# Performance work log

Measured on AMD Instinct MI355X. Metric: run time of the kernel, lower is better.

Reference implementation:

```python
import jax, jax.numpy as jnp
import numpy as np

S, B, H = 2048, 2, 1024
NH = 16
HD = H // NH  # 64


def setup_inputs() -> dict:
    key = jax.random.key(0)
    k1, k2 = jax.random.split(key)
    hidden_states = jax.random.normal(k1, (S, B, H), dtype=jnp.float32)
    W_qkv = jax.random.normal(k2, (3 * H, H), dtype=jnp.float32) * (H ** -0.5)
    b_qkv = jnp.zeros((3 * H,), dtype=jnp.float32)
    return {"hidden_states": hidden_states, "W_qkv": W_qkv, "b_qkv": b_qkv}


def reference(hidden_states, W_qkv, b_qkv):
    s, b, h = hidden_states.shape
    # QKV projection: [S,B,3H] -> [S,B,NH,3*HD] -> split
    qkv = hidden_states @ W_qkv.T + b_qkv
    qkv = qkv.reshape(s, b, NH, 3 * HD)
    q, k, v = jnp.split(qkv, 3, axis=-1)  # each [S,B,NH,HD]
    norm_factor = HD ** -0.5
    # scores: [B,NH,Sq,Sk]
    scores = jnp.einsum('sbhd,tbhd->bhst', q, k) * norm_factor
    # Cumsum sequence-op (seq_op_in_fp32=True): cumsum over key dim, scaled by Sq^-0.5
    probs = jnp.cumsum(scores.astype(jnp.float32), axis=-1) * (s ** -0.5)
    probs = probs.astype(hidden_states.dtype)
    # PV: [B,NH,Sq,HD] -> seq-first [Sq,B,NH*HD]
    ctx = jnp.einsum('bhst,tbhd->sbhd', probs, v)
    return ctx.reshape(s, b, h)
```

## Files before the change

### kernel.cpp

```cpp
#include <hip/hip_runtime.h>

#define S 2048
#define B 2
#define H 1024
#define NH 16
#define HD 64
#define THREE_H 3072
#define ROWS (S*B)

typedef __attribute__((ext_vector_type(8))) short short8;
typedef __attribute__((ext_vector_type(4))) float f32x4;
typedef const __attribute__((address_space(1))) unsigned int* gptr_t;
typedef __attribute__((address_space(3))) unsigned int* lptr_t;

#define N8_A (ROWS * H / 8)
#define N8_W (THREE_H * H / 8)

__device__ __forceinline__ ushort f2bf(float f) {
    union { float f; unsigned u; } v; v.f = f;
    unsigned r = v.u + 0x7fffu + ((v.u >> 16) & 1u);
    return (ushort)(r >> 16);
}
__device__ __forceinline__ float bf2f(ushort u) {
    union { unsigned u; float f; } v; v.u = ((unsigned)u) << 16;
    return v.f;
}

__global__ void cast_both(const float* __restrict__ A, const float* __restrict__ W,
                          ushort* __restrict__ Ab, ushort* __restrict__ Wb) {
    int i = blockIdx.x * 256 + threadIdx.x;
    const float4* s4;
    ushort* dst;
    if (i < N8_A) { s4 = (const float4*)A; dst = Ab; }
    else if (i < N8_A + N8_W) { s4 = (const float4*)W; dst = Wb; i -= N8_A; }
    else return;
    float4 a = s4[2 * i], b = s4[2 * i + 1];
    short8 o;
    o[0] = f2bf(a.x); o[1] = f2bf(a.y); o[2] = f2bf(a.z); o[3] = f2bf(a.w);
    o[4] = f2bf(b.x); o[5] = f2bf(b.y); o[6] = f2bf(b.z); o[7] = f2bf(b.w);
    *(short8*)(dst + 8 * (size_t)i) = o;
}

__global__ __launch_bounds__(512) void qkv_gemm_mfma(const ushort* __restrict__ Abf,
                                                     const ushort* __restrict__ Wbf,
                                                     const float* __restrict__ bias,
                                                     ushort* __restrict__ Qb,
                                                     ushort* __restrict__ Ktd,
                                                     ushort* __restrict__ Vtd) {
    __shared__ ushort Abuf[128 * 32];
    __shared__ ushort Bbuf[128 * 32];
    const int tid = threadIdx.x;
    const int wave = tid >> 6, lane = tid & 63;
    const int wr = wave >> 1, wc = wave & 1;
    const int row0 = blockIdx.x * 128;
    const int col0 = blockIdx.y * 128;

    f32x4 acc[2][4] = {};

    const int lrow = lane >> 2;
    const int gk = ((lane & 3) ^ ((lrow >> 1) & 3)) * 8;
    const int il = lane & 15, ko = lane >> 4;

    for (int k0 = 0; k0 < H; k0 += 32) {
        {
            int row = wave * 16 + lrow;
            __builtin_amdgcn_global_load_lds(
                (gptr_t)&Abf[(size_t)(row0 + row) * H + k0 + gk],
                (lptr_t)&Abuf[wave * 512 + lane * 8], 16, 0, 0);
            __builtin_amdgcn_global_load_lds(
                (gptr_t)&Wbf[(size_t)(col0 + row) * H + k0 + gk],
                (lptr_t)&Bbuf[wave * 512 + lane * 8], 16, 0, 0);
        }
        __syncthreads();

        short8 af[2], bfr[4];
#pragma unroll
        for (int m = 0; m < 2; ++m) {
            int ar = wr * 32 + m * 16 + il;
            af[m] = *(const short8*)&Abuf[ar * 32 + (ko ^ ((ar >> 1) & 3)) * 8];
        }
#pragma unroll
        for (int n = 0; n < 4; ++n) {
            int br = wc * 64 + n * 16 + il;
            bfr[n] = *(const short8*)&Bbuf[br * 32 + (ko ^ ((br >> 1) & 3)) * 8];
        }
#pragma unroll
        for (int m = 0; m < 2; ++m)
#pragma unroll
            for (int n = 0; n < 4; ++n)
                acc[m][n] = __builtin_amdgcn_mfma_f32_16x16x32_bf16(af[m], bfr[n], acc[m][n], 0, 0, 0);
        __syncthreads();
    }

#pragma unroll
    for (int n = 0; n < 4; ++n) {
        int cbase = col0 + wc * 64 + n * 16;
        int h   = cbase / 192;
        int r3  = cbase % 192;
        int sel = r3 >> 6;
        int d   = (r3 & 63) + il;
        float bv = bias[cbase + il];
        if (sel == 0) {
#pragma unroll
            for (int m = 0; m < 2; ++m) {
                int rowb = row0 + wr * 32 + m * 16 + ko * 4;
#pragma unroll
                for (int j = 0; j < 4; ++j) {
                    int r = rowb + j;
                    int s = r >> 1, b = r & 1;
                    Qb[((size_t)((b * NH + h) * S + s)) * HD + d] = f2bf(acc[m][n][j] + bv);
                }
            }
        } else {
            ushort* dst = (sel == 1) ? Ktd : Vtd;
            const size_t ro0 = ((size_t)(h)      * HD + d) * S;
            const size_t ro1 = ((size_t)(NH + h) * HD + d) * S;
#pragma unroll
            for (int m = 0; m < 2; ++m) {
                int t0 = (row0 + wr * 32 + m * 16 + ko * 4) >> 1;
                uint lo = (uint)f2bf(acc[m][n][0] + bv) |
                          ((uint)f2bf(acc[m][n][2] + bv) << 16);
                uint hi = (uint)f2bf(acc[m][n][1] + bv) |
                          ((uint)f2bf(acc[m][n][3] + bv) << 16);
                *(uint*)&dst[ro0 + t0] = lo;
                *(uint*)&dst[ro1 + t0] = hi;
            }
        }
    }
}

__global__ __launch_bounds__(256) void vscan(ushort* __restrict__ Vtd) {
    const int row = blockIdx.x * 4 + (threadIdx.x >> 6);
    const int lane = threadIdx.x & 63;
    ushort* vp = Vtd + (size_t)row * S + lane * 32;
    float v[32];
#pragma unroll
    for (int q = 0; q < 4; ++q) {
        short8 x = *(const short8*)(vp + q * 8);
#pragma unroll
        for (int k = 0; k < 8; ++k) v[q * 8 + k] = bf2f((ushort)x[k]);
    }
    float sum = 0.f;
#pragma unroll
    for (int k = 0; k < 32; ++k) sum += v[k];
    float t = sum;
#pragma unroll
    for (int off = 1; off < 64; off <<= 1) {
        float o = __shfl_down(t, off, 64);
        if (lane + off < 64) t += o;
    }
    float acc = t - sum;
#pragma unroll
    for (int k = 31; k >= 0; --k) { acc += v[k]; v[k] = acc; }
#pragma unroll
    for (int q = 0; q < 4; ++q) {
        short8 o;
#pragma unroll
        for (int k = 0; k < 8; ++k) o[k] = f2bf(v[q * 8 + k]);
        *(short8*)(vp + q * 8) = o;
    }
}

__global__ __launch_bounds__(256) void kvm_mfma(const ushort* __restrict__ Kt,
                                                const ushort* __restrict__ Vt,
                                                float* __restrict__ Mpart) {
    __shared__ float red[2][4096];
    const int bh = blockIdx.x, kb = blockIdx.y;
    const int tid = threadIdx.x, wave = tid >> 6, lane = tid & 63;
    const int slice = kb * 4 + wave;
    const ushort* Kp = Kt + (size_t)bh * HD * S;
    const ushort* Vp = Vt + (size_t)bh * HD * S;
    f32x4 acc[4][4] = {};
    const int il = lane & 15, g = lane >> 4;
    const int tbase = slice * 128 + g * 8;
#pragma unroll
    for (int ks = 0; ks < 4; ++ks) {
        const int t = tbase + ks * 32;
        short8 af[4], bfv[4];
#pragma unroll
        for (int m = 0; m < 4; ++m) af[m]  = *(const short8*)&Kp[(size_t)(m * 16 + il) * S + t];
#pragma unroll
        for (int n = 0; n < 4; ++n) bfv[n] = *(const short8*)&Vp[(size_t)(n * 16 + il) * S + t];
#pragma unroll
        for (int m = 0; m < 4; ++m)
#pragma unroll
            for (int n = 0; n < 4; ++n)
                acc[m][n] = __builtin_amdgcn_mfma_f32_16x16x32_bf16(af[m], bfv[n], acc[m][n], 0, 0, 0);
    }
#define DUMP(dstbuf)                                                        \
    { float* _d = (dstbuf);                                                 \
      _Pragma("unroll") for (int m = 0; m < 4; ++m)                         \
      _Pragma("unroll") for (int n = 0; n < 4; ++n)                         \
      _Pragma("unroll") for (int j = 0; j < 4; ++j)                         \
          _d[(m * 16 + g * 4 + j) * 64 + n * 16 + il] = acc[m][n][j]; }
#define ADDIN(srcbuf)                                                       \
    { const float* _s = (srcbuf);                                           \
      _Pragma("unroll") for (int m = 0; m < 4; ++m)                         \
      _Pragma("unroll") for (int n = 0; n < 4; ++n)                         \
      _Pragma("unroll") for (int j = 0; j < 4; ++j)                         \
          acc[m][n][j] += _s[(m * 16 + g * 4 + j) * 64 + n * 16 + il]; }
    if (wave == 1) DUMP(red[0]);
    if (wave == 3) DUMP(red[1]);
    __syncthreads();
    if (wave == 0) ADDIN(red[0]);
    if (wave == 2) ADDIN(red[1]);
    __syncthreads();
    if (wave == 2) DUMP(red[0]);
    __syncthreads();
    if (wave == 0) {
        ADDIN(red[0]);
        float* Mp = Mpart + ((size_t)kb * 32 + bh) * 4096;
#pragma unroll
        for (int m = 0; m < 4; ++m)
#pragma unroll
            for (int n = 0; n < 4; ++n)
#pragma unroll
                for (int j = 0; j < 4; ++j)
                    Mp[(m * 16 + g * 4 + j) * 64 + n * 16 + il] = acc[m][n][j];
    }
#undef DUMP
#undef ADDIN
}

__global__ __launch_bounds__(256) void qm_mfma(const ushort* __restrict__ Qb,
                                               const float* __restrict__ Mpart,
                                               float* __restrict__ out) {
    __shared__ ushort Mt[64][72];
    const int bh = blockIdx.x, b = bh >> 4, h = bh & 15;
    const int tid = threadIdx.x;
    {
        const int i = tid >> 2, jq = (tid & 3) * 16;
        f32x4 s0 = {}, s1 = {}, s2 = {}, s3 = {};
#pragma unroll
        for (int sl = 0; sl < 4; ++sl) {
            const float* p = Mpart + ((size_t)sl * 32 + bh) * 4096 + i * 64 + jq;
            s0 += *(const f32x4*)(p);
            s1 += *(const f32x4*)(p + 4);
            s2 += *(const f32x4*)(p + 8);
            s3 += *(const f32x4*)(p + 12);
        }
#pragma unroll
        for (int k = 0; k < 4; ++k) {
            Mt[jq + 0  + k][i] = f2bf(s0[k]);
            Mt[jq + 4  + k][i] = f2bf(s1[k]);
            Mt[jq + 8  + k][i] = f2bf(s2[k]);
            Mt[jq + 12 + k][i] = f2bf(s3[k]);
        }
    }
    __syncthreads();
    const int wave = tid >> 6, lane = tid & 63;
    const int sl15 = lane & 15, koct = (lane >> 4) * 8;
    const int s0b = blockIdx.y * 256 + wave * 64;
    f32x4 acc[4][4] = {};
#pragma unroll
    for (int ks = 0; ks < 2; ++ks) {
        short8 af[4], bfv[4];
#pragma unroll
        for (int m = 0; m < 4; ++m) {
            int s = s0b + m * 16 + sl15;
            af[m] = *(const short8*)&Qb[((size_t)bh * S + s) * HD + ks * 32 + koct];
        }
#pragma unroll
        for (int n = 0; n < 4; ++n)
            bfv[n] = *(const short8*)&Mt[n * 16 + sl15][ks * 32 + koct];
#pragma unroll
        for (int m = 0; m < 4; ++m)
#pragma unroll
            for (int n = 0; n < 4; ++n)
                acc[m][n] = __builtin_amdgcn_mfma_f32_16x16x32_bf16(af[m], bfv[n], acc[m][n], 0, 0, 0);
    }
    const float scale = 0.125f * 0.02209708691207961f;
#pragma unroll
    for (int m = 0; m < 4; ++m)
#pragma unroll
        for (int n = 0; n < 4; ++n)
#pragma unroll
            for (int j = 0; j < 4; ++j) {
                int s = s0b + m * 16 + (lane >> 4) * 4 + j;
                int d = n * 16 + sl15;
                out[(size_t)(s * B + b) * H + h * 64 + d] = acc[m][n][j] * scale;
            }
}

extern "C" void kernel_launch(void* const* d_in, const int* in_sizes, int n_in,
                              void* d_out, int out_size, void* d_ws, size_t ws_size,
                              hipStream_t stream) {
    const float* hidden = (const float*)d_in[0];
    const float* W      = (const float*)d_in[1];
    const float* bias   = (const float*)d_in[2];
    float* out = (float*)d_out;

    ushort* Qb    = (ushort*)d_ws;
    ushort* Ktd   = Qb + 4194304;
    ushort* Vtd   = Ktd + 4194304;
    float*  Mpart = (float*)(Vtd + 4194304);
    ushort* Abf   = (ushort*)(Mpart + 524288);
    ushort* Wbf   = Abf + 4194304;

    cast_both<<<(N8_A + N8_W + 255) / 256, 256, 0, stream>>>(hidden, W, Abf, Wbf);
    qkv_gemm_mfma<<<dim3(ROWS / 128, THREE_H / 128), 512, 0, stream>>>(Abf, Wbf, bias, Qb, Ktd, Vtd);
    vscan<<<512, 256, 0, stream>>>(Vtd);
    kvm_mfma<<<dim3(32, 4), 256, 0, stream>>>(Ktd, Vtd, Mpart);
    qm_mfma<<<dim3(32, 8), 256, 0, stream>>>(Qb, Mpart, out);
}
```

Before: 70.93 us.

## Double-buffer QKV GEMM LDS tiles with BK=64 and async prefetch

Restructures the QKV projection GEMM main loop to use two LDS buffers with a 64-wide K tile, issuing global-to-LDS loads two stages ahead and waiting with explicit vmcnt counts instead of a full sync each step. The swizzle is changed to an 8-way XOR over the wider rows, and MFMA sections get raised wave priority. This is meant to overlap memory latency with matrix math and halve the number of barriers. In exchange it quadruples the LDS footprint, which may reduce occupancy, and relies on hand-counted waitcnt correctness.

```diff
diff --git a/kernel.cpp b/kernel.cpp
--- a/kernel.cpp
+++ b/kernel.cpp
@@ -47,8 +47,8 @@
                                                      ushort* __restrict__ Qb,
                                                      ushort* __restrict__ Ktd,
                                                      ushort* __restrict__ Vtd) {
-    __shared__ ushort Abuf[128 * 32];
-    __shared__ ushort Bbuf[128 * 32];
+    __shared__ ushort Abuf[2][128 * 64];
+    __shared__ ushort Bbuf[2][128 * 64];
     const int tid = threadIdx.x;
     const int wave = tid >> 6, lane = tid & 63;
     const int wr = wave >> 1, wc = wave & 1;
@@ -57,40 +57,67 @@
 
     f32x4 acc[2][4] = {};
 
-    const int lrow = lane >> 2;
-    const int gk = ((lane & 3) ^ ((lrow >> 1) & 3)) * 8;
+    const int srow = lane >> 3;
+    const int gk = ((lane & 7) ^ srow) * 8;
     const int il = lane & 15, ko = lane >> 4;
 
-    for (int k0 = 0; k0 < H; k0 += 32) {
-        {
-            int row = wave * 16 + lrow;
-            __builtin_amdgcn_global_load_lds(
-                (gptr_t)&Abf[(size_t)(row0 + row) * H + k0 + gk],
-                (lptr_t)&Abuf[wave * 512 + lane * 8], 16, 0, 0);
-            __builtin_amdgcn_global_load_lds(
-                (gptr_t)&Wbf[(size_t)(col0 + row) * H + k0 + gk],
-                (lptr_t)&Bbuf[wave * 512 + lane * 8], 16, 0, 0);
-        }
-        __syncthreads();
-
-        short8 af[2], bfr[4];
-#pragma unroll
-        for (int m = 0; m < 2; ++m) {
-            int ar = wr * 32 + m * 16 + il;
-            af[m] = *(const short8*)&Abuf[ar * 32 + (ko ^ ((ar >> 1) & 3)) * 8];
-        }
-#pragma unroll
-        for (int n = 0; n < 4; ++n) {
-            int br = wc * 64 + n * 16 + il;
-            bfr[n] = *(const short8*)&Bbuf[br * 32 + (ko ^ ((br >> 1) & 3)) * 8];
-        }
-#pragma unroll
-        for (int m = 0; m < 2; ++m)
-#pragma unroll
-            for (int n = 0; n < 4; ++n)
-                acc[m][n] = __builtin_amdgcn_mfma_f32_16x16x32_bf16(af[m], bfr[n], acc[m][n], 0, 0, 0);
-        __syncthreads();
-    }
+    const size_t arow0 = (size_t)(row0 + wave * 16 + srow) * H + gk;
+    const size_t arow1 = arow0 + (size_t)8 * H;
+    const size_t wrow0 = (size_t)(col0 + wave * 16 + srow) * H + gk;
+    const size_t wrow1 = wrow0 + (size_t)8 * H;
+    const int ld0 = (wave * 16) * 64 + lane * 8;
+    const int ld1 = ld0 + 8 * 64;
+
+#define STAGE(buf, k0)                                                        \
+    {                                                                         \
+        __builtin_amdgcn_global_load_lds((gptr_t)&Abf[arow0 + (k0)],          \
+            (lptr_t)&Abuf[buf][ld0], 16, 0, 0);                               \
+        __builtin_amdgcn_global_load_lds((gptr_t)&Wbf[wrow0 + (k0)],          \
+            (lptr_t)&Bbuf[buf][ld0], 16, 0, 0);                               \
+        __builtin_amdgcn_global_load_lds((gptr_t)&Abf[arow1 + (k0)],          \
+            (lptr_t)&Abuf[buf][ld1], 16, 0, 0);                               \
+        __builtin_amdgcn_global_load_lds((gptr_t)&Wbf[wrow1 + (k0)],          \
+            (lptr_t)&Bbuf[buf][ld1], 16, 0, 0);                               \
+    }
+
+    STAGE(0, 0);
+    STAGE(1, 64);
+
+    int cur = 0;
+    for (int t = 0; t < 16; ++t) {
+        if (t < 15) { asm volatile("s_waitcnt vmcnt(4)" ::: "memory"); }
+        else        { asm volatile("s_waitcnt vmcnt(0)" ::: "memory"); }
+        __builtin_amdgcn_s_barrier();
+        __builtin_amdgcn_sched_barrier(0);
+
+#pragma unroll
+        for (int kh = 0; kh < 2; ++kh) {
+            short8 af[2], bfr[4];
+#pragma unroll
+            for (int m = 0; m < 2; ++m) {
+                int ar = wr * 32 + m * 16 + il;
+                af[m] = *(const short8*)&Abuf[cur][ar * 64 + ((kh * 4 + ko) ^ (ar & 7)) * 8];
+            }
+#pragma unroll
+            for (int n = 0; n < 4; ++n) {
+                int br = wc * 64 + n * 16 + il;
+                bfr[n] = *(const short8*)&Bbuf[cur][br * 64 + ((kh * 4 + ko) ^ (br & 7)) * 8];
+            }
+            __builtin_amdgcn_s_setprio(1);
+#pragma unroll
+            for (int m = 0; m < 2; ++m)
+#pragma unroll
+                for (int n = 0; n < 4; ++n)
+                    acc[m][n] = __builtin_amdgcn_mfma_f32_16x16x32_bf16(af[m], bfr[n], acc[m][n], 0, 0, 0);
+            __builtin_amdgcn_s_setprio(0);
+        }
+
+        __builtin_amdgcn_s_barrier();
+        __builtin_amdgcn_sched_barrier(0);
+        if (t < 14) STAGE(cur, (t + 2) * 64);
+        cur ^= 1;
+    }
+#undef STAGE
 
 #pragma unroll
     for (int n = 0; n < 4; ++n) {
```

Result: slower. 75.24 us (+6.1%).

## Fuse fp32-to-bf16 cast into QKV GEMM with register-prefetched global loads

Applied to the files above, without the earlier changes.

Removes the separate cast kernel and its bf16 staging buffers. The GEMM now reads fp32 activations and weights directly, converts them with packed bf16 conversion instructions, and writes them to LDS. The next K-slice is prefetched into registers while the current one is computed, and MFMA priority is raised. The cost is that the GEMM reads twice the bytes per tile, and each W tile is re-read as fp32 by many blocks. The per-iteration conversion and explicit barriers add instruction overhead.

```diff
diff --git a/kernel.cpp b/kernel.cpp
--- a/kernel.cpp
+++ b/kernel.cpp
@@ -10,11 +10,9 @@
 
 typedef __attribute__((ext_vector_type(8))) short short8;
 typedef __attribute__((ext_vector_type(4))) float f32x4;
+typedef __attribute__((ext_vector_type(4))) uint uint4v;
 typedef const __attribute__((address_space(1))) unsigned int* gptr_t;
 typedef __attribute__((address_space(3))) unsigned int* lptr_t;
-
-#define N8_A (ROWS * H / 8)
-#define N8_W (THREE_H * H / 8)
 
 __device__ __forceinline__ ushort f2bf(float f) {
     union { float f; unsigned u; } v; v.f = f;
@@ -25,24 +23,14 @@
     union { unsigned u; float f; } v; v.u = ((unsigned)u) << 16;
     return v.f;
 }
-
-__global__ void cast_both(const float* __restrict__ A, const float* __restrict__ W,
-                          ushort* __restrict__ Ab, ushort* __restrict__ Wb) {
-    int i = blockIdx.x * 256 + threadIdx.x;
-    const float4* s4;
-    ushort* dst;
-    if (i < N8_A) { s4 = (const float4*)A; dst = Ab; }
-    else if (i < N8_A + N8_W) { s4 = (const float4*)W; dst = Wb; i -= N8_A; }
-    else return;
-    float4 a = s4[2 * i], b = s4[2 * i + 1];
-    short8 o;
-    o[0] = f2bf(a.x); o[1] = f2bf(a.y); o[2] = f2bf(a.z); o[3] = f2bf(a.w);
-    o[4] = f2bf(b.x); o[5] = f2bf(b.y); o[6] = f2bf(b.z); o[7] = f2bf(b.w);
-    *(short8*)(dst + 8 * (size_t)i) = o;
-}
-
-__global__ __launch_bounds__(512) void qkv_gemm_mfma(const ushort* __restrict__ Abf,
-                                                     const ushort* __restrict__ Wbf,
+__device__ __forceinline__ uint cvtpk(float lo, float hi) {
+    uint r;
+    asm volatile("v_cvt_pk_bf16_f32 %0, %1, %2" : "=v"(r) : "v"(lo), "v"(hi));
+    return r;
+}
+
+__global__ __launch_bounds__(512) void qkv_gemm_mfma(const float* __restrict__ Af,
+                                                     const float* __restrict__ Wf,
                                                      const float* __restrict__ bias,
                                                      ushort* __restrict__ Qb,
                                                      ushort* __restrict__ Ktd,
@@ -58,20 +46,40 @@
     f32x4 acc[2][4] = {};
 
     const int lrow = lane >> 2;
-    const int gk = ((lane & 3) ^ ((lrow >> 1) & 3)) * 8;
+    const int gko = (lane & 3) ^ ((lrow >> 1) & 3);
     const int il = lane & 15, ko = lane >> 4;
 
-    for (int k0 = 0; k0 < H; k0 += 32) {
+    const float* aP = Af + (size_t)(row0 + wave * 16 + lrow) * H + gko * 8;
+    const float* wP = Wf + (size_t)(col0 + wave * 16 + lrow) * H + gko * 8;
+
+    f32x4 aLo = *(const f32x4*)(aP), aHi = *(const f32x4*)(aP + 4);
+    f32x4 wLo = *(const f32x4*)(wP), wHi = *(const f32x4*)(wP + 4);
+
+    uint* adst = (uint*)&Abuf[wave * 512 + lane * 8];
+    uint* bdst = (uint*)&Bbuf[wave * 512 + lane * 8];
+
+    for (int t = 0; t < 32; ++t) {
+        __builtin_amdgcn_s_barrier();
+        __builtin_amdgcn_sched_barrier(0);
         {
-            int row = wave * 16 + lrow;
-            __builtin_amdgcn_global_load_lds(
-                (gptr_t)&Abf[(size_t)(row0 + row) * H + k0 + gk],
-                (lptr_t)&Abuf[wave * 512 + lane * 8], 16, 0, 0);
-            __builtin_amdgcn_global_load_lds(
-                (gptr_t)&Wbf[(size_t)(col0 + row) * H + k0 + gk],
-                (lptr_t)&Bbuf[wave * 512 + lane * 8], 16, 0, 0);
-        }
-        __syncthreads();
+            uint4v pa, pw;
+            pa.x = cvtpk(aLo.x, aLo.y); pa.y = cvtpk(aLo.z, aLo.w);
+            pa.z = cvtpk(aHi.x, aHi.y); pa.w = cvtpk(aHi.z, aHi.w);
+            pw.x = cvtpk(wLo.x, wLo.y); pw.y = cvtpk(wLo.z, wLo.w);
+            pw.z = cvtpk(wHi.x, wHi.y); pw.w = cvtpk(wHi.z, wHi.w);
+            *(uint4v*)adst = pa;
+            *(uint4v*)bdst = pw;
+        }
+        asm volatile("s_waitcnt lgkmcnt(0)" ::: "memory");
+        if (t < 31) {
+            const float* ap = aP + (t + 1) * 32;
+            const float* wp = wP + (t + 1) * 32;
+            aLo = *(const f32x4*)(ap); aHi = *(const f32x4*)(ap + 4);
+            wLo = *(const f32x4*)(wp); wHi = *(const f32x4*)(wp + 4);
+        }
+        __builtin_amdgcn_sched_barrier(0);
+        __builtin_amdgcn_s_barrier();
+        __builtin_amdgcn_sched_barrier(0);
 
         short8 af[2], bfr[4];
 #pragma unroll
@@ -84,12 +92,13 @@
             int br = wc * 64 + n * 16 + il;
             bfr[n] = *(const short8*)&Bbuf[br * 32 + (ko ^ ((br >> 1) & 3)) * 8];
         }
+        __builtin_amdgcn_s_setprio(1);
 #pragma unroll
         for (int m = 0; m < 2; ++m)
 #pragma unroll
             for (int n = 0; n < 4; ++n)
                 acc[m][n] = __builtin_amdgcn_mfma_f32_16x16x32_bf16(af[m], bfr[n], acc[m][n], 0, 0, 0);
-        __syncthreads();
+        __builtin_amdgcn_s_setprio(0);
     }
 
 #pragma unroll
@@ -294,11 +303,8 @@
     ushort* Ktd   = Qb + 4194304;
     ushort* Vtd   = Ktd + 4194304;
     float*  Mpart = (float*)(Vtd + 4194304);
-    ushort* Abf   = (ushort*)(Mpart + 524288);
-    ushort* Wbf   = Abf + 4194304;
-
-    cast_both<<<(N8_A + N8_W + 255) / 256, 256, 0, stream>>>(hidden, W, Abf, Wbf);
-    qkv_gemm_mfma<<<dim3(ROWS / 128, THREE_H / 128), 512, 0, stream>>>(Abf, Wbf, bias, Qb, Ktd, Vtd);
+
+    qkv_gemm_mfma<<<dim3(ROWS / 128, THREE_H / 128), 512, 0, stream>>>(hidden, W, bias, Qb, Ktd, Vtd);
     vscan<<<512, 256, 0, stream>>>(Vtd);
     kvm_mfma<<<dim3(32, 4), 256, 0, stream>>>(Ktd, Vtd, Mpart);
     qm_mfma<<<dim3(32, 8), 256, 0, stream>>>(Qb, Mpart, out);
```

New measurement: 73.69 us. +3.9%, slower.

## Fuse K^T·V reduction and Q·M product into one kernel with recomputation

Applied to the files above, without the earlier changes.

Merges the kernel that builds the per-head 64x64 K^T·V state with the kernel that multiplies Q by that state. Each block now computes the full state over all keys with 8 waves, reduces it in shared memory, converts it to bf16 and uses it directly. This removes one launch and the partial-sum round trip through global memory. In exchange, each of the 8 sequence blocks per head recomputes the same state, multiplying the K/V reads and MFMA work for that stage.

```diff
diff --git a/kernel.cpp b/kernel.cpp
--- a/kernel.cpp
+++ b/kernel.cpp
@@ -161,32 +161,38 @@
     }
 }
 
-__global__ __launch_bounds__(256) void kvm_mfma(const ushort* __restrict__ Kt,
-                                                const ushort* __restrict__ Vt,
-                                                float* __restrict__ Mpart) {
-    __shared__ float red[2][4096];
-    const int bh = blockIdx.x, kb = blockIdx.y;
+__global__ __launch_bounds__(512) void kvqm_fused(const ushort* __restrict__ Kt,
+                                                  const ushort* __restrict__ Vt,
+                                                  const ushort* __restrict__ Qb,
+                                                  float* __restrict__ out) {
+    __shared__ float red[4][4096];
+    __shared__ ushort Mt[64][72];
+    const int bh = blockIdx.x, sb = blockIdx.y;
+    const int b = bh >> 4, h = bh & 15;
     const int tid = threadIdx.x, wave = tid >> 6, lane = tid & 63;
-    const int slice = kb * 4 + wave;
+    const int il = lane & 15, g = lane >> 4;
     const ushort* Kp = Kt + (size_t)bh * HD * S;
     const ushort* Vp = Vt + (size_t)bh * HD * S;
+
     f32x4 acc[4][4] = {};
-    const int il = lane & 15, g = lane >> 4;
-    const int tbase = slice * 128 + g * 8;
-#pragma unroll
-    for (int ks = 0; ks < 4; ++ks) {
-        const int t = tbase + ks * 32;
-        short8 af[4], bfv[4];
-#pragma unroll
-        for (int m = 0; m < 4; ++m) af[m]  = *(const short8*)&Kp[(size_t)(m * 16 + il) * S + t];
-#pragma unroll
-        for (int n = 0; n < 4; ++n) bfv[n] = *(const short8*)&Vp[(size_t)(n * 16 + il) * S + t];
-#pragma unroll
-        for (int m = 0; m < 4; ++m)
-#pragma unroll
-            for (int n = 0; n < 4; ++n)
-                acc[m][n] = __builtin_amdgcn_mfma_f32_16x16x32_bf16(af[m], bfv[n], acc[m][n], 0, 0, 0);
-    }
+    {
+        const int tbase = wave * 256 + g * 8;
+#pragma unroll
+        for (int ks = 0; ks < 8; ++ks) {
+            const int t = tbase + ks * 32;
+            short8 af[4], bfv[4];
+#pragma unroll
+            for (int m = 0; m < 4; ++m) af[m]  = *(const short8*)&Kp[(size_t)(m * 16 + il) * S + t];
+#pragma unroll
+            for (int n = 0; n < 4; ++n) bfv[n] = *(const short8*)&Vp[(size_t)(n * 16 + il) * S + t];
+#pragma unroll
+            for (int m = 0; m < 4; ++m)
+#pragma unroll
+                for (int n = 0; n < 4; ++n)
+                    acc[m][n] = __builtin_amdgcn_mfma_f32_16x16x32_bf16(af[m], bfv[n], acc[m][n], 0, 0, 0);
+        }
+    }
+
 #define DUMP(dstbuf)                                                        \
     { float* _d = (dstbuf);                                                 \
       _Pragma("unroll") for (int m = 0; m < 4; ++m)                         \
@@ -199,86 +205,59 @@
       _Pragma("unroll") for (int n = 0; n < 4; ++n)                         \
       _Pragma("unroll") for (int j = 0; j < 4; ++j)                         \
           acc[m][n][j] += _s[(m * 16 + g * 4 + j) * 64 + n * 16 + il]; }
+    if (wave >= 4) DUMP(red[wave - 4]);
+    __syncthreads();
+    if (wave < 4) ADDIN(red[wave]);
+    __syncthreads();
+    if (wave == 2 || wave == 3) DUMP(red[wave - 2]);
+    __syncthreads();
+    if (wave < 2) ADDIN(red[wave]);
+    __syncthreads();
     if (wave == 1) DUMP(red[0]);
-    if (wave == 3) DUMP(red[1]);
-    __syncthreads();
-    if (wave == 0) ADDIN(red[0]);
-    if (wave == 2) ADDIN(red[1]);
-    __syncthreads();
-    if (wave == 2) DUMP(red[0]);
     __syncthreads();
     if (wave == 0) {
         ADDIN(red[0]);
-        float* Mp = Mpart + ((size_t)kb * 32 + bh) * 4096;
 #pragma unroll
         for (int m = 0; m < 4; ++m)
 #pragma unroll
             for (int n = 0; n < 4; ++n)
 #pragma unroll
                 for (int j = 0; j < 4; ++j)
-                    Mp[(m * 16 + g * 4 + j) * 64 + n * 16 + il] = acc[m][n][j];
-    }
+                    Mt[n * 16 + il][m * 16 + g * 4 + j] = f2bf(acc[m][n][j]);
+    }
+    __syncthreads();
 #undef DUMP
 #undef ADDIN
-}
-
-__global__ __launch_bounds__(256) void qm_mfma(const ushort* __restrict__ Qb,
-                                               const float* __restrict__ Mpart,
-                                               float* __restrict__ out) {
-    __shared__ ushort Mt[64][72];
-    const int bh = blockIdx.x, b = bh >> 4, h = bh & 15;
-    const int tid = threadIdx.x;
-    {
-        const int i = tid >> 2, jq = (tid & 3) * 16;
-        f32x4 s0 = {}, s1 = {}, s2 = {}, s3 = {};
-#pragma unroll
-        for (int sl = 0; sl < 4; ++sl) {
-            const float* p = Mpart + ((size_t)sl * 32 + bh) * 4096 + i * 64 + jq;
-            s0 += *(const f32x4*)(p);
-            s1 += *(const f32x4*)(p + 4);
-            s2 += *(const f32x4*)(p + 8);
-            s3 += *(const f32x4*)(p + 12);
-        }
-#pragma unroll
-        for (int k = 0; k < 4; ++k) {
-            Mt[jq + 0  + k][i] = f2bf(s0[k]);
-            Mt[jq + 4  + k][i] = f2bf(s1[k]);
-            Mt[jq + 8  + k][i] = f2bf(s2[k]);
-            Mt[jq + 12 + k][i] = f2bf(s3[k]);
-        }
-    }
-    __syncthreads();
-    const int wave = tid >> 6, lane = tid & 63;
-    const int sl15 = lane & 15, koct = (lane >> 4) * 8;
-    const int s0b = blockIdx.y * 256 + wave * 64;
-    f32x4 acc[4][4] = {};
+
+    const int s0b = sb * 256 + wave * 32;
+    f32x4 qacc[2][4] = {};
 #pragma unroll
     for (int ks = 0; ks < 2; ++ks) {
-        short8 af[4], bfv[4];
-#pragma unroll
-        for (int m = 0; m < 4; ++m) {
-            int s = s0b + m * 16 + sl15;
-            af[m] = *(const short8*)&Qb[((size_t)bh * S + s) * HD + ks * 32 + koct];
+        short8 af[2], bfv[4];
+#pragma unroll
+        for (int m = 0; m < 2; ++m) {
+            int s = s0b + m * 16 + il;
+            af[m] = *(const short8*)&Qb[((size_t)bh * S + s) * HD + ks * 32 + g * 8];
         }
 #pragma unroll
         for (int n = 0; n < 4; ++n)
-            bfv[n] = *(const short8*)&Mt[n * 16 + sl15][ks * 32 + koct];
-#pragma unroll
-        for (int m = 0; m < 4; ++m)
+            bfv[n] = *(const short8*)&Mt[n * 16 + il][ks * 32 + g * 8];
+#pragma unroll
+        for (int m = 0; m < 2; ++m)
 #pragma unroll
             for (int n = 0; n < 4; ++n)
-                acc[m][n] = __builtin_amdgcn_mfma_f32_16x16x32_bf16(af[m], bfv[n], acc[m][n], 0, 0, 0);
+                qacc[m][n] = __builtin_amdgcn_mfma_f32_16x16x32_bf16(af[m], bfv[n], qacc[m][n], 0, 0, 0);
     }
     const float scale = 0.125f * 0.02209708691207961f;
 #pragma unroll
-    for (int m = 0; m < 4; ++m)
+    for (int m = 0; m < 2; ++m)
 #pragma unroll
         for (int n = 0; n < 4; ++n)
 #pragma unroll
             for (int j = 0; j < 4; ++j) {
-                int s = s0b + m * 16 + (lane >> 4) * 4 + j;
-                int d = n * 16 + sl15;
-                out[(size_t)(s * B + b) * H + h * 64 + d] = acc[m][n][j] * scale;
+                int s = s0b + m * 16 + g * 4 + j;
+                int d = n * 16 + il;
+                out[(size_t)(s * B + b) * H + h * 64 + d] = qacc[m][n][j] * scale;
             }
 }
 
@@ -293,13 +272,11 @@
     ushort* Qb    = (ushort*)d_ws;
     ushort* Ktd   = Qb + 4194304;
     ushort* Vtd   = Ktd + 4194304;
-    float*  Mpart = (float*)(Vtd + 4194304);
-    ushort* Abf   = (ushort*)(Mpart + 524288);
+    ushort* Abf   = Vtd + 4194304;
     ushort* Wbf   = Abf + 4194304;
 
     cast_both<<<(N8_A + N8_W + 255) / 256, 256, 0, stream>>>(hidden, W, Abf, Wbf);
     qkv_gemm_mfma<<<dim3(ROWS / 128, THREE_H / 128), 512, 0, stream>>>(Abf, Wbf, bias, Qb, Ktd, Vtd);
     vscan<<<512, 256, 0, stream>>>(Vtd);
-    kvm_mfma<<<dim3(32, 4), 256, 0, stream>>>(Ktd, Vtd, Mpart);
-    qm_mfma<<<dim3(32, 8), 256, 0, stream>>>(Qb, Mpart, out);
-}
+    kvqm_fused<<<dim3(32, 8), 512, 0, stream>>>(Ktd, Vtd, Qb, out);
+}
```

New measurement: 77.00 us. +8.6%, slower.
